# Kernel tuning notes

Hardware: AMD Instinct MI355X
Metric: run time of the kernel (lower is better)

Reference implementation:

```python
import jax, jax.numpy as jnp
import numpy as np

B, T, D, E, FF, K = 4, 1024, 1024, 8, 2048, 2
SINKHORN_ITERS = 3


def setup_inputs() -> dict:
    key = jax.random.key(0)
    ks = jax.random.split(key, 7)
    scale = 0.02
    return {
        "x": jax.random.normal(ks[0], (B, T, D), dtype=jnp.float32),
        "router_w": jax.random.normal(ks[1], (E, D), dtype=jnp.float32) * scale,  # nn.Linear(D,E).weight
        "router_b": jnp.zeros((E,), dtype=jnp.float32),
        "temperature": jnp.ones((1,), dtype=jnp.float32) * 0.5,
        "wg": jax.random.normal(ks[2], (E, D, FF), dtype=jnp.float32) * scale,   # expert gate weights
        "wp": jax.random.normal(ks[3], (E, D, FF), dtype=jnp.float32) * scale,   # expert proj weights
        "wo": jax.random.normal(ks[4], (E, FF, D), dtype=jnp.float32) * scale,   # expert out_proj weights
    }


def _sinkhorn(log_alpha, iters=SINKHORN_ITERS):
    for _ in range(iters):
        log_alpha = log_alpha - jax.nn.logsumexp(log_alpha, axis=-1, keepdims=True)
        log_alpha = log_alpha - jax.nn.logsumexp(log_alpha, axis=-2, keepdims=True)
    gates = jnp.exp(log_alpha)
    return gates / (jnp.sum(gates, axis=-1, keepdims=True) + 1e-8)


def reference(x, router_w, router_b, temperature, wg, wp, wo):
    # Router scores with clamped temperature (clamp(min=0.1))
    temp = jnp.maximum(temperature, 0.1)
    scores = (jnp.einsum("btd,ed->bte", x, router_w) + router_b) / temp  # [B,T,E]

    # T>1 and E>1 -> Sinkhorn doubly-stochastic normalization
    gates = _sinkhorn(scores)

    topk_vals, topk_idx = jax.lax.top_k(gates, K)                 # [B,T,K]
    topk_gates = topk_vals / (jnp.sum(topk_vals, axis=-1, keepdims=True) + 1e-8)

    # Dense all-expert FFN (relu-gated GLU), matching mask-and-sum semantics.
    # sum_k sum_i (idx_k==i)*gate_k*expert_i(x) == sum_k gate_k * expert_{idx_k}(x)
    g = jax.nn.relu(jnp.einsum("btd,edf->btef", x, wg))           # [B,T,E,FF]
    p = jnp.einsum("btd,edf->btef", x, wp)                        # [B,T,E,FF]
    all_out = jnp.einsum("btef,efd->bted", g * p, wo)             # [B,T,E,D]

    gathered = jnp.take_along_axis(all_out, topk_idx[..., None], axis=2)  # [B,T,K,D]
    expert_out = jnp.sum(gathered * topk_gates[..., None], axis=2)        # [B,T,D]

    return x + expert_out
```

## Files before the change

### kernel.cpp

```cpp
#include <hip/hip_runtime.h>
#include <hip/hip_bf16.h>
#include <stdint.h>

#define B_   4
#define T_   1024
#define D_   1024
#define E_   8
#define FF_  2048
#define NT_  4096
#define LCAP 9472
#define NTS1 (D_ / 64)
#define NT2  (FF_ / 32)

typedef unsigned short u16;
typedef __attribute__((ext_vector_type(8))) short bf16x8;
typedef __attribute__((ext_vector_type(4))) float f32x4;

#define MFMA16(a, b, c) __builtin_amdgcn_mfma_f32_16x16x32_bf16((a), (b), (c), 0, 0, 0)

__device__ __forceinline__ u16 f2bf(float f) {
  union { float f; uint32_t u; } c; c.f = f;
  return (u16)((c.u + 0x7FFFu + ((c.u >> 16) & 1u)) >> 16);
}

__device__ __forceinline__ void gl_lds16(const void* g, void* l) {
  __builtin_amdgcn_global_load_lds(
      (const __attribute__((address_space(1))) uint32_t*)g,
      (__attribute__((address_space(3))) uint32_t*)l, 16, 0, 0);
}


__global__ __launch_bounds__(256) void k_init(int* __restrict__ tok, float* __restrict__ gate,
                                              int* __restrict__ cnt, int* __restrict__ cur) {
  int i = blockIdx.x * 256 + threadIdx.x;
  if (i < LCAP) { tok[i] = 0; gate[i] = 0.f; }
  if (i < E_)   { cnt[i] = 0; cur[i] = 0; }
}

__global__ __launch_bounds__(256) void k_router(const float* __restrict__ x,
                                                const float* __restrict__ rw,
                                                const float* __restrict__ rb,
                                                const float* __restrict__ temp,
                                                float* __restrict__ scores,
                                                float* __restrict__ out,
                                                u16* __restrict__ xb) {
  int wid  = (blockIdx.x * 256 + threadIdx.x) >> 6;
  int lane = threadIdx.x & 63;
  const float* xr = x + (size_t)wid * D_;
  float* orow = out + (size_t)wid * D_;
  u16* xrow = xb + (size_t)wid * D_;
  float acc[E_];
  #pragma unroll
  for (int e = 0; e < E_; ++e) acc[e] = 0.f;
  for (int i = lane; i < D_; i += 64) {
    float xv = xr[i];
    orow[i] = xv;
    xrow[i] = f2bf(xv);
    #pragma unroll
    for (int e = 0; e < E_; ++e) acc[e] += xv * rw[e * D_ + i];
  }
  float inv = 1.0f / fmaxf(temp[0], 0.1f);
  #pragma unroll
  for (int e = 0; e < E_; ++e) {
    float v = acc[e];
    for (int off = 32; off; off >>= 1) v += __shfl_xor(v, off);
    if (lane == 0) scores[(size_t)wid * E_ + e] = (v + rb[e]) * inv;
  }
}

__global__ __launch_bounds__(1024) void k_sinkhorn(const float* __restrict__ scores,
                                                   float* __restrict__ tkg, int* __restrict__ tki,
                                                   int* __restrict__ cnt) {
  const int b = blockIdx.x, t = threadIdx.x;
  const int row = b * T_ + t;
  float s[E_];
  #pragma unroll
  for (int e = 0; e < E_; ++e) s[e] = scores[(size_t)row * E_ + e];

  __shared__ float red[16][E_];
  __shared__ int lcnt[E_];
  if (t < E_) lcnt[t] = 0;
  const int wid = t >> 6, lane = t & 63;

  for (int it = 0; it < 3; ++it) {
    float m = s[0];
    #pragma unroll
    for (int e = 1; e < E_; ++e) m = fmaxf(m, s[e]);
    float sum = 0.f;
    #pragma unroll
    for (int e = 0; e < E_; ++e) sum += expf(s[e] - m);
    float lse = m + logf(sum);
    #pragma unroll
    for (int e = 0; e < E_; ++e) s[e] -= lse;

    float cm[E_];
    #pragma unroll
    for (int e = 0; e < E_; ++e) {
      float v = s[e];
      for (int off = 32; off; off >>= 1) v = fmaxf(v, __shfl_xor(v, off));
      if (lane == 0) red[wid][e] = v;
    }
    __syncthreads();
    #pragma unroll
    for (int e = 0; e < E_; ++e) {
      float mm = red[0][e];
      for (int wv = 1; wv < 16; ++wv) mm = fmaxf(mm, red[wv][e]);
      cm[e] = mm;
    }
    __syncthreads();
    #pragma unroll
    for (int e = 0; e < E_; ++e) {
      float v = expf(s[e] - cm[e]);
      for (int off = 32; off; off >>= 1) v += __shfl_xor(v, off);
      if (lane == 0) red[wid][e] = v;
    }
    __syncthreads();
    #pragma unroll
    for (int e = 0; e < E_; ++e) {
      float ss = 0.f;
      for (int wv = 0; wv < 16; ++wv) ss += red[wv][e];
      s[e] -= cm[e] + logf(ss);
    }
    __syncthreads();
  }

  float g[E_]; float rs = 0.f;
  #pragma unroll
  for (int e = 0; e < E_; ++e) { g[e] = expf(s[e]); rs += g[e]; }
  float inv = 1.f / (rs + 1e-8f);
  #pragma unroll
  for (int e = 0; e < E_; ++e) g[e] *= inv;

  int i0 = 0; float v0 = g[0];
  #pragma unroll
  for (int e = 1; e < E_; ++e) if (g[e] > v0) { v0 = g[e]; i0 = e; }
  int i1 = -1; float v1 = -1e30f;
  #pragma unroll
  for (int e = 0; e < E_; ++e) if (e != i0 && g[e] > v1) { v1 = g[e]; i1 = e; }
  float den = 1.f / (v0 + v1 + 1e-8f);
  tkg[row * 2 + 0] = v0 * den; tki[row * 2 + 0] = i0;
  tkg[row * 2 + 1] = v1 * den; tki[row * 2 + 1] = i1;

  atomicAdd(&lcnt[i0], 1);
  atomicAdd(&lcnt[i1], 1);
  __syncthreads();
  if (t < E_) atomicAdd(&cnt[t], lcnt[t]);
}

__global__ void k_offsets(const int* __restrict__ cnt, int* __restrict__ segoff) {
  if (threadIdx.x == 0 && blockIdx.x == 0) {
    int run = 0;
    for (int e = 0; e < E_; ++e) { segoff[e] = run; run += ((cnt[e] + 127) >> 7) << 7; }
    segoff[E_] = run;
  }
}

__global__ __launch_bounds__(256) void k_scatter(const int* __restrict__ tki, const float* __restrict__ tkg,
                                                 const int* __restrict__ segoff, int* __restrict__ cur,
                                                 int* __restrict__ tok, float* __restrict__ gate) {
  int idx = blockIdx.x * 256 + threadIdx.x;
  int row = idx >> 1;
  int e = tki[idx];
  float g = tkg[idx];
  int pos = atomicAdd(&cur[e], 1);
  int p = segoff[e] + pos;
  tok[p] = row;
  gate[p] = g;
}

__global__ __launch_bounds__(256) void k_transpose(const float* __restrict__ in, u16* __restrict__ out,
                                                   int R, int C) {
  __shared__ __align__(16) u16 t[32][36];
  const size_t msz = (size_t)R * C;
  const float* A = in + blockIdx.z * msz;
  u16* O = out + blockIdx.z * msz;
  const int r0 = blockIdx.y * 32, c0 = blockIdx.x * 32;
  const int tid = threadIdx.x;
  {
    const int i = tid >> 3, j4 = (tid & 7) << 2;
    const float4 v = *(const float4*)(A + (size_t)(r0 + i) * C + c0 + j4);
    ushort4 pk; pk.x = f2bf(v.x); pk.y = f2bf(v.y); pk.z = f2bf(v.z); pk.w = f2bf(v.w);
    *(ushort4*)(&t[i][j4]) = pk;
  }
  __syncthreads();
  {
    const int j2 = tid & 15;
    #pragma unroll
    for (int it = 0; it < 2; ++it) {
      const int r = (tid >> 4) + it * 16;
      uint32_t pv = (uint32_t)t[2 * j2][r] | ((uint32_t)t[2 * j2 + 1][r] << 16);
      *(uint32_t*)(O + (size_t)(c0 + r) * R + r0 + 2 * j2) = pv;
    }
  }
}

__global__ __launch_bounds__(256) void k_transpose_w(const float* __restrict__ in,
                                                     u16* __restrict__ out, int woff) {
  __shared__ __align__(16) u16 t[32][36];
  const float* A = in + (size_t)blockIdx.z * D_ * FF_;
  u16* O = out + (size_t)blockIdx.z * 4096 * 1024;
  const int r0 = blockIdx.y * 32, c0 = blockIdx.x * 32;
  const int tid = threadIdx.x;
  {
    const int i = tid >> 3, j4 = (tid & 7) << 2;
    const float4 v = *(const float4*)(A + (size_t)(r0 + i) * FF_ + c0 + j4);
    ushort4 pk; pk.x = f2bf(v.x); pk.y = f2bf(v.y); pk.z = f2bf(v.z); pk.w = f2bf(v.w);
    *(ushort4*)(&t[i][j4]) = pk;
  }
  __syncthreads();
  {
    const int j2 = tid & 15;
    #pragma unroll
    for (int it = 0; it < 2; ++it) {
      const int r = (tid >> 4) + it * 16;
      const int f = c0 + r;
      const int fp = ((f >> 4) << 5) + (f & 15) + woff;
      uint32_t pv = (uint32_t)t[2 * j2][r] | ((uint32_t)t[2 * j2 + 1][r] << 16);
      *(uint32_t*)(O + (size_t)fp * 1024 + r0 + 2 * j2) = pv;
    }
  }
}


__global__ __launch_bounds__(512, 2) void k_stage1(
    const u16* __restrict__ wa, const u16* __restrict__ xb,
    const int* __restrict__ tok, const int* __restrict__ segoff,
    u16* __restrict__ H) {
  const int raw = blockIdx.x;
  const int e   = raw & 7;
  const int rem = raw >> 3;
  const int ft  = rem >> 4;
  const int pt2 = rem & 15;
  const int seg0 = segoff[e], segend = segoff[e + 1];
  if (pt2 * 256 >= segend - seg0) return;
  const int tid = threadIdx.x;
  const int lane = tid & 63;
  const int w = tid >> 6;
  const int lane15 = lane & 15, lchunk = lane >> 4;
  const int lk8 = lchunk * 8;
  const int fw = w >> 2, pw = w & 3;

  __shared__ __align__(16) u16 LA[2][16384];
  __shared__ __align__(16) u16 LB[2][16384];

  const int prow0 = seg0 + pt2 * 256;
  const u16* asrc0 = wa + (size_t)e * 4096 * 1024
                        + (size_t)(ft * 256 + 2 * w * 16 + lane15) * 1024 + lk8;
  const u16* asrc1 = asrc0 + 16 * 1024;
  const int tk0 = tok[prow0 + 2 * w * 16 + lane15];
  const int tk1 = tok[prow0 + 2 * w * 16 + 16 + lane15];
  const u16* bsrc0 = xb + (size_t)tk0 * D_ + lk8;
  const u16* bsrc1 = xb + (size_t)tk1 * D_ + lk8;
  const int dA0 = 2 * w * 512, dA1 = dA0 + 512;

  const f32x4 vz = {0.f, 0.f, 0.f, 0.f};
  f32x4 acc[8][4];
  #pragma unroll
  for (int m = 0; m < 8; ++m)
    #pragma unroll
    for (int n = 0; n < 4; ++n) acc[m][n] = vz;

#define STG_A(c, s) do { const int o_ = (s) * 64;           \
    gl_lds16(asrc0 + o_,      &LA[c][dA0]);                 \
    gl_lds16(asrc0 + o_ + 32, &LA[c][dA0 + 8192]);          \
    gl_lds16(asrc1 + o_,      &LA[c][dA1]);                 \
    gl_lds16(asrc1 + o_ + 32, &LA[c][dA1 + 8192]); } while (0)
#define STG_B(c, s) do { const int o_ = (s) * 64;           \
    gl_lds16(bsrc0 + o_,      &LB[c][dA0]);                 \
    gl_lds16(bsrc0 + o_ + 32, &LB[c][dA0 + 8192]);          \
    gl_lds16(bsrc1 + o_,      &LB[c][dA1]);                 \
    gl_lds16(bsrc1 + o_ + 32, &LB[c][dA1 + 8192]); } while (0)

  STG_A(0, 0); STG_B(0, 0);
  #pragma unroll 1
  for (int s = 0; s < NTS1; ++s) {
    const int c = s & 1;
    asm volatile("s_waitcnt vmcnt(0)" ::: "memory");
    __builtin_amdgcn_s_barrier();
    asm volatile("" ::: "memory");
    const u16* la = LA[c];
    const u16* lb = LB[c];
    bf16x8 bv[4][2];
    #pragma unroll
    for (int n = 0; n < 4; ++n)
      #pragma unroll
      for (int kc = 0; kc < 2; ++kc)
        bv[n][kc] = *(const bf16x8*)(lb + kc * 8192 + (pw * 4 + n) * 512 + lane * 8);
    #pragma unroll
    for (int p = 0; p < 4; ++p) {
      bf16x8 av[2][2];
      #pragma unroll
      for (int mm = 0; mm < 2; ++mm)
        #pragma unroll
        for (int kc = 0; kc < 2; ++kc)
          av[mm][kc] = *(const bf16x8*)(la + kc * 8192 + (fw * 8 + 2 * p + mm) * 512 + lane * 8);
      if (p == 0) { if (s + 1 < NTS1) STG_A(c ^ 1, s + 1); }
      if (p == 1) { if (s + 1 < NTS1) STG_B(c ^ 1, s + 1); }
      __builtin_amdgcn_s_setprio(1);
      #pragma unroll
      for (int mm = 0; mm < 2; ++mm)
        #pragma unroll
        for (int n = 0; n < 4; ++n)
          #pragma unroll
          for (int kc = 0; kc < 2; ++kc)
            acc[2 * p + mm][n] = MFMA16(av[mm][kc], bv[n][kc], acc[2 * p + mm][n]);
      __builtin_amdgcn_s_setprio(0);
      if (p < 3) {
        __builtin_amdgcn_s_barrier();
        asm volatile("" ::: "memory");
      }
    }
  }
#undef STG_A
#undef STG_B

  const int jrow = lchunk * 4;
  #pragma unroll
  for (int q = 0; q < 4; ++q) {
    const int fcol = ft * 128 + fw * 64 + q * 16 + jrow;
    #pragma unroll
    for (int n = 0; n < 4; ++n) {
      const int prow = prow0 + pw * 64 + n * 16 + lane15;
      if (prow < segend) {
        union { uint2 v; u16 s[4]; } u;
        #pragma unroll
        for (int j = 0; j < 4; ++j)
          u.s[j] = f2bf(fmaxf(acc[2 * q][n][j], 0.f) * acc[2 * q + 1][n][j]);
        *(uint2*)(H + (size_t)prow * FF_ + fcol) = u.v;
      }
    }
  }
}

__global__ __launch_bounds__(512, 4) void k_stage2(
    const u16* __restrict__ H, const u16* __restrict__ woT,
    const int* __restrict__ tok, const float* __restrict__ gate,
    const int* __restrict__ cnt, const int* __restrict__ segoff,
    float* __restrict__ out) {
  const int raw = blockIdx.x;
  const int e   = raw & 7;
  const int rem = raw >> 3;
  const int dt  = rem >> 5;
  const int pt  = rem & 31;
  if (pt * 128 >= cnt[e]) return;
  const int tid = threadIdx.x;
  const int lane = tid & 63;
  const int w = tid >> 6;
  const int lane15 = lane & 15, lchunk = lane >> 4;
  const int ph = w >> 2, dq = w & 3;

  __shared__ __align__(16) u16 LH[3][4096];
  __shared__ __align__(16) u16 LW[3][4096];
  __shared__ int   ltok[128];
  __shared__ float lgt[128];

  const int prow0 = segoff[e] + pt * 128;
  if (tid < 128) { ltok[tid] = tok[prow0 + tid]; lgt[tid] = gate[prow0 + tid]; }

  const u16* hsrc = H + (size_t)(prow0 + w * 16 + lane15) * FF_ + lchunk * 8;
  const u16* wsrc = woT + (size_t)e * D_ * FF_
                        + (size_t)(dt * 128 + w * 16 + lane15) * FF_ + lchunk * 8;
  const int dstb = w * 512;

  const f32x4 vz = {0.f, 0.f, 0.f, 0.f};
  f32x4 acc[4][2];
  #pragma unroll
  for (int m = 0; m < 4; ++m)
    #pragma unroll
    for (int n = 0; n < 2; ++n) acc[m][n] = vz;

#define ISSUE2(c, t) do { const int o_ = (t) * 32;                 \
    gl_lds16(hsrc + o_, &LH[c][dstb]);                             \
    gl_lds16(wsrc + o_, &LW[c][dstb]); } while (0)

#define COMP2(c) do {                                                        \
    const u16* lh = LH[c]; const u16* lw = LW[c];                            \
    bf16x8 ah[4], bw[2];                                                     \
    _Pragma("unroll")                                                        \
    for (int m = 0; m < 4; ++m)                                              \
      ah[m] = *(const bf16x8*)(lh + (ph * 4 + m) * 512 + lane * 8);          \
    _Pragma("unroll")                                                        \
    for (int n = 0; n < 2; ++n)                                              \
      bw[n] = *(const bf16x8*)(lw + (dq * 2 + n) * 512 + lane * 8);          \
    __builtin_amdgcn_s_setprio(1);                                           \
    _Pragma("unroll")                                                        \
    for (int m = 0; m < 4; ++m)                                              \
      _Pragma("unroll")                                                      \
      for (int n = 0; n < 2; ++n)                                            \
        acc[m][n] = MFMA16(ah[m], bw[n], acc[m][n]);                         \
    __builtin_amdgcn_s_setprio(0); } while (0)

  ISSUE2(0, 0);
  ISSUE2(1, 1);
  #pragma unroll 1
  for (int t = 0; t < NT2 - 1; ++t) {
    asm volatile("s_waitcnt vmcnt(2)" ::: "memory");
    __builtin_amdgcn_s_barrier();
    asm volatile("" ::: "memory");
    if (t + 2 < NT2) { const int cn = (t + 2) % 3; ISSUE2(cn, t + 2); }
    const int c = t % 3;
    COMP2(c);
  }
  asm volatile("s_waitcnt vmcnt(0)" ::: "memory");
  __builtin_amdgcn_s_barrier();
  asm volatile("" ::: "memory");
  COMP2((NT2 - 1) % 3);
#undef ISSUE2
#undef COMP2

  const int jrow = lchunk * 4;
  #pragma unroll
  for (int m = 0; m < 4; ++m) {
    #pragma unroll
    for (int n = 0; n < 2; ++n) {
      const int dcol = dt * 128 + dq * 32 + n * 16 + lane15;
      #pragma unroll
      for (int j = 0; j < 4; ++j) {
        const int pl = ph * 64 + m * 16 + jrow + j;
        unsafeAtomicAdd(&out[(size_t)ltok[pl] * D_ + dcol], lgt[pl] * acc[m][n][j]);
      }
    }
  }
}


extern "C" void kernel_launch(void* const* d_in, const int* in_sizes, int n_in,
                              void* d_out, int out_size, void* d_ws, size_t ws_size,
                              hipStream_t stream) {
  const float* x    = (const float*)d_in[0];
  const float* rw   = (const float*)d_in[1];
  const float* rb   = (const float*)d_in[2];
  const float* temp = (const float*)d_in[3];
  const float* wg   = (const float*)d_in[4];
  const float* wp   = (const float*)d_in[5];
  const float* wo   = (const float*)d_in[6];
  float* out = (float*)d_out;
  char* ws = (char*)d_ws;

  const size_t O_XB  = 0;
  const size_t O_WA  = 8388608;
  const size_t O_WOT = O_WA;
  const size_t O_H   = O_WA + 67108864;
  const size_t O_SC  = O_H + (size_t)LCAP * FF_ * 2;
  const size_t O_TKG = O_SC + (size_t)NT_ * E_ * 4;
  const size_t O_TKI = O_TKG + (size_t)NT_ * 2 * 4;
  const size_t O_CNT = O_TKI + (size_t)NT_ * 2 * 4;
  const size_t O_CUR = O_CNT + 128;
  const size_t O_SEG = O_CUR + 128;
  const size_t O_TOK = O_SEG + 128;
  const size_t O_GTE = O_TOK + (size_t)LCAP * 4;
  const size_t REQ   = O_GTE + (size_t)LCAP * 4;
  if (ws_size < REQ) return;

  u16*   xb     = (u16*)(ws + O_XB);
  u16*   wa     = (u16*)(ws + O_WA);
  u16*   woT    = (u16*)(ws + O_WOT);
  u16*   Hbuf   = (u16*)(ws + O_H);
  float* scores = (float*)(ws + O_SC);
  float* tkg    = (float*)(ws + O_TKG);
  int*   tki    = (int*)(ws + O_TKI);
  int*   cnt    = (int*)(ws + O_CNT);
  int*   cur    = (int*)(ws + O_CUR);
  int*   segoff = (int*)(ws + O_SEG);
  int*   tok    = (int*)(ws + O_TOK);
  float* gate   = (float*)(ws + O_GTE);

  k_init<<<(LCAP + 255) / 256, 256, 0, stream>>>(tok, gate, cnt, cur);
  k_router<<<NT_ / 4, 256, 0, stream>>>(x, rw, rb, temp, scores, out, xb);
  k_sinkhorn<<<B_, 1024, 0, stream>>>(scores, tkg, tki, cnt);
  k_offsets<<<1, 64, 0, stream>>>(cnt, segoff);
  k_scatter<<<(NT_ * 2) / 256, 256, 0, stream>>>(tki, tkg, segoff, cur, tok, gate);

  k_transpose_w<<<dim3(FF_ / 32, D_ / 32, E_), 256, 0, stream>>>(wg, wa, 0);
  k_transpose_w<<<dim3(FF_ / 32, D_ / 32, E_), 256, 0, stream>>>(wp, wa, 16);

  k_stage1<<<16 * 16 * E_, 512, 0, stream>>>(wa, xb, tok, segoff, Hbuf);

  k_transpose<<<dim3(D_ / 32, FF_ / 32, E_), 256, 0, stream>>>(wo, woT, FF_, D_);

  k_stage2<<<32 * 8 * E_, 512, 0, stream>>>(Hbuf, woT, tok, gate, cnt, segoff, out);
}
```

Baseline: 471.4 us.

## Fuse init into router, merge weight transposes with 128x128 tiles, trim sinkhorn reductions

Folds the workspace-init kernel into the router kernel and merges the wg/wp transpose launches into one kernel. The transposes now use 128x128 LDS tiles with 16-byte stores, replacing 32x32 tiles with 4-byte stores, to get better-coalesced writes of the bf16 weight copies. The Sinkhorn column reductions are also computed once by 8 threads and broadcast through shared memory instead of every thread re-reducing. The trade is larger LDS tiles, which may reduce occupancy, scattered 2-byte LDS writes that may bank-conflict, and two extra barriers per Sinkhorn iteration.

Measured after the change: 463.3 us. Within noise of the previous version (-1.7%).

```diff
diff --git a/kernel.cpp b/kernel.cpp
--- a/kernel.cpp
+++ b/kernel.cpp
@@ -30,21 +30,20 @@
 }
 
 
-__global__ __launch_bounds__(256) void k_init(int* __restrict__ tok, float* __restrict__ gate,
-                                              int* __restrict__ cnt, int* __restrict__ cur) {
-  int i = blockIdx.x * 256 + threadIdx.x;
-  if (i < LCAP) { tok[i] = 0; gate[i] = 0.f; }
-  if (i < E_)   { cnt[i] = 0; cur[i] = 0; }
-}
-
 __global__ __launch_bounds__(256) void k_router(const float* __restrict__ x,
                                                 const float* __restrict__ rw,
                                                 const float* __restrict__ rb,
                                                 const float* __restrict__ temp,
                                                 float* __restrict__ scores,
                                                 float* __restrict__ out,
-                                                u16* __restrict__ xb) {
-  int wid  = (blockIdx.x * 256 + threadIdx.x) >> 6;
+                                                u16* __restrict__ xb,
+                                                int* __restrict__ tok, float* __restrict__ gate,
+                                                int* __restrict__ cnt, int* __restrict__ cur) {
+  const int gid = blockIdx.x * 256 + threadIdx.x;
+  if (gid < LCAP) { tok[gid] = 0; gate[gid] = 0.f; }
+  if (gid < E_)   { cnt[gid] = 0; cur[gid] = 0; }
+
+  int wid  = gid >> 6;
   int lane = threadIdx.x & 63;
   const float* xr = x + (size_t)wid * D_;
   float* orow = out + (size_t)wid * D_;
@@ -78,6 +77,7 @@
   for (int e = 0; e < E_; ++e) s[e] = scores[(size_t)row * E_ + e];
 
   __shared__ float red[16][E_];
+  __shared__ float redv[E_];
   __shared__ int lcnt[E_];
   if (t < E_) lcnt[t] = 0;
   const int wid = t >> 6, lane = t & 63;
@@ -93,7 +93,6 @@
     #pragma unroll
     for (int e = 0; e < E_; ++e) s[e] -= lse;
 
-    float cm[E_];
     #pragma unroll
     for (int e = 0; e < E_; ++e) {
       float v = s[e];
@@ -101,13 +100,17 @@
       if (lane == 0) red[wid][e] = v;
     }
     __syncthreads();
-    #pragma unroll
-    for (int e = 0; e < E_; ++e) {
-      float mm = red[0][e];
-      for (int wv = 1; wv < 16; ++wv) mm = fmaxf(mm, red[wv][e]);
-      cm[e] = mm;
+    if (t < E_) {
+      float mm = red[0][t];
+      #pragma unroll
+      for (int wv = 1; wv < 16; ++wv) mm = fmaxf(mm, red[wv][t]);
+      redv[t] = mm;
     }
     __syncthreads();
+    float cm[E_];
+    #pragma unroll
+    for (int e = 0; e < E_; ++e) cm[e] = redv[e];
+
     #pragma unroll
     for (int e = 0; e < E_; ++e) {
       float v = expf(s[e] - cm[e]);
@@ -115,12 +118,15 @@
       if (lane == 0) red[wid][e] = v;
     }
     __syncthreads();
-    #pragma unroll
-    for (int e = 0; e < E_; ++e) {
+    if (t < E_) {
       float ss = 0.f;
-      for (int wv = 0; wv < 16; ++wv) ss += red[wv][e];
-      s[e] -= cm[e] + logf(ss);
-    }
+      #pragma unroll
+      for (int wv = 0; wv < 16; ++wv) ss += red[wv][t];
+      redv[t] = ss;
+    }
+    __syncthreads();
+    #pragma unroll
+    for (int e = 0; e < E_; ++e) s[e] -= cm[e] + logf(redv[e]);
     __syncthreads();
   }
 
@@ -168,57 +174,63 @@
   gate[p] = g;
 }
 
-__global__ __launch_bounds__(256) void k_transpose(const float* __restrict__ in, u16* __restrict__ out,
-                                                   int R, int C) {
-  __shared__ __align__(16) u16 t[32][36];
-  const size_t msz = (size_t)R * C;
-  const float* A = in + blockIdx.z * msz;
-  u16* O = out + blockIdx.z * msz;
-  const int r0 = blockIdx.y * 32, c0 = blockIdx.x * 32;
+
+__global__ __launch_bounds__(256) void k_transpose_wgp(const float* __restrict__ wg,
+                                                       const float* __restrict__ wp,
+                                                       u16* __restrict__ wa) {
+  __shared__ __align__(16) u16 ldsT[128][136];
+  const int e = blockIdx.z >> 1, iswp = blockIdx.z & 1;
+  const float* src = (iswp ? wp : wg) + (size_t)e * D_ * FF_;
+  const int woff = iswp * 16;
+  const int f0 = blockIdx.x * 128, d0 = blockIdx.y * 128;
   const int tid = threadIdx.x;
-  {
-    const int i = tid >> 3, j4 = (tid & 7) << 2;
-    const float4 v = *(const float4*)(A + (size_t)(r0 + i) * C + c0 + j4);
-    ushort4 pk; pk.x = f2bf(v.x); pk.y = f2bf(v.y); pk.z = f2bf(v.z); pk.w = f2bf(v.w);
-    *(ushort4*)(&t[i][j4]) = pk;
+  #pragma unroll
+  for (int it = 0; it < 16; ++it) {
+    const int fi = it * 256 + tid;
+    const int rowd = fi >> 5;
+    const int col4 = fi & 31;
+    const float4 v = *(const float4*)(src + (size_t)(d0 + rowd) * FF_ + f0 + col4 * 4);
+    ldsT[col4 * 4 + 0][rowd] = f2bf(v.x);
+    ldsT[col4 * 4 + 1][rowd] = f2bf(v.y);
+    ldsT[col4 * 4 + 2][rowd] = f2bf(v.z);
+    ldsT[col4 * 4 + 3][rowd] = f2bf(v.w);
   }
   __syncthreads();
-  {
-    const int j2 = tid & 15;
-    #pragma unroll
-    for (int it = 0; it < 2; ++it) {
-      const int r = (tid >> 4) + it * 16;
-      uint32_t pv = (uint32_t)t[2 * j2][r] | ((uint32_t)t[2 * j2 + 1][r] << 16);
-      *(uint32_t*)(O + (size_t)(c0 + r) * R + r0 + 2 * j2) = pv;
-    }
-  }
-}
-
-__global__ __launch_bounds__(256) void k_transpose_w(const float* __restrict__ in,
-                                                     u16* __restrict__ out, int woff) {
-  __shared__ __align__(16) u16 t[32][36];
-  const float* A = in + (size_t)blockIdx.z * D_ * FF_;
-  u16* O = out + (size_t)blockIdx.z * 4096 * 1024;
-  const int r0 = blockIdx.y * 32, c0 = blockIdx.x * 32;
+  const int cl = tid >> 1, half = tid & 1;
+  const int f = f0 + cl;
+  const int fp = ((f >> 4) << 5) + (f & 15) + woff;
+  u16* dst = wa + (size_t)e * 4096 * 1024 + (size_t)fp * 1024 + d0 + half * 64;
+  const u16* srcl = &ldsT[cl][half * 64];
+  #pragma unroll
+  for (int i = 0; i < 8; ++i)
+    *(uint4*)(dst + i * 8) = *(const uint4*)(srcl + i * 8);
+}
+
+__global__ __launch_bounds__(256) void k_transpose_wo(const float* __restrict__ wo,
+                                                      u16* __restrict__ woT) {
+  __shared__ __align__(16) u16 ldsT[128][136];
+  const int e = blockIdx.z;
+  const float* src = wo + (size_t)e * FF_ * D_;
+  const int d0 = blockIdx.x * 128, ff0 = blockIdx.y * 128;
   const int tid = threadIdx.x;
-  {
-    const int i = tid >> 3, j4 = (tid & 7) << 2;
-    const float4 v = *(const float4*)(A + (size_t)(r0 + i) * FF_ + c0 + j4);
-    ushort4 pk; pk.x = f2bf(v.x); pk.y = f2bf(v.y); pk.z = f2bf(v.z); pk.w = f2bf(v.w);
-    *(ushort4*)(&t[i][j4]) = pk;
+  #pragma unroll
+  for (int it = 0; it < 16; ++it) {
+    const int fi = it * 256 + tid;
+    const int rowf = fi >> 5;
+    const int col4 = fi & 31;
+    const float4 v = *(const float4*)(src + (size_t)(ff0 + rowf) * D_ + d0 + col4 * 4);
+    ldsT[col4 * 4 + 0][rowf] = f2bf(v.x);
+    ldsT[col4 * 4 + 1][rowf] = f2bf(v.y);
+    ldsT[col4 * 4 + 2][rowf] = f2bf(v.z);
+    ldsT[col4 * 4 + 3][rowf] = f2bf(v.w);
   }
   __syncthreads();
-  {
-    const int j2 = tid & 15;
-    #pragma unroll
-    for (int it = 0; it < 2; ++it) {
-      const int r = (tid >> 4) + it * 16;
-      const int f = c0 + r;
-      const int fp = ((f >> 4) << 5) + (f & 15) + woff;
-      uint32_t pv = (uint32_t)t[2 * j2][r] | ((uint32_t)t[2 * j2 + 1][r] << 16);
-      *(uint32_t*)(O + (size_t)fp * 1024 + r0 + 2 * j2) = pv;
-    }
-  }
+  const int dl = tid >> 1, half = tid & 1;
+  u16* dst = woT + (size_t)e * D_ * FF_ + (size_t)(d0 + dl) * FF_ + ff0 + half * 64;
+  const u16* srcl = &ldsT[dl][half * 64];
+  #pragma unroll
+  for (int i = 0; i < 8; ++i)
+    *(uint4*)(dst + i * 8) = *(const uint4*)(srcl + i * 8);
 }
 
 
@@ -465,18 +477,17 @@
   int*   tok    = (int*)(ws + O_TOK);
   float* gate   = (float*)(ws + O_GTE);
 
-  k_init<<<(LCAP + 255) / 256, 256, 0, stream>>>(tok, gate, cnt, cur);
-  k_router<<<NT_ / 4, 256, 0, stream>>>(x, rw, rb, temp, scores, out, xb);
+  k_router<<<NT_ / 4, 256, 0, stream>>>(x, rw, rb, temp, scores, out, xb,
+                                        tok, gate, cnt, cur);
   k_sinkhorn<<<B_, 1024, 0, stream>>>(scores, tkg, tki, cnt);
   k_offsets<<<1, 64, 0, stream>>>(cnt, segoff);
   k_scatter<<<(NT_ * 2) / 256, 256, 0, stream>>>(tki, tkg, segoff, cur, tok, gate);
 
-  k_transpose_w<<<dim3(FF_ / 32, D_ / 32, E_), 256, 0, stream>>>(wg, wa, 0);
-  k_transpose_w<<<dim3(FF_ / 32, D_ / 32, E_), 256, 0, stream>>>(wp, wa, 16);
+  k_transpose_wgp<<<dim3(FF_ / 128, D_ / 128, E_ * 2), 256, 0, stream>>>(wg, wp, wa);
 
   k_stage1<<<16 * 16 * E_, 512, 0, stream>>>(wa, xb, tok, segoff, Hbuf);
 
-  k_transpose<<<dim3(D_ / 32, FF_ / 32, E_), 256, 0, stream>>>(wo, woT, FF_, D_);
+  k_transpose_wo<<<dim3(D_ / 128, FF_ / 128, E_), 256, 0, stream>>>(wo, woT);
 
   k_stage2<<<32 * 8 * E_, 512, 0, stream>>>(Hbuf, woT, tok, gate, cnt, segoff, out);
 }
```
